# Optimization experiments

Hardware: AMD Instinct MI355X
Metric: run time of the kernel (lower is better)

Reference implementation:

```python
import jax, jax.numpy as jnp
import numpy as np

N_NODES, N_EDGES, FEA_DIM, H_DIM, N_LAYER, N_GRAPHS, LABEL_DIM = 50000, 600000, 128, 256, 3, 256, 2


def setup_inputs() -> dict:
    key = jax.random.key(0)
    ks = jax.random.split(key, 8)
    x = jax.random.normal(ks[0], (N_NODES, FEA_DIM), jnp.float32)
    edge_index = jax.random.randint(ks[1], (2, N_EDGES), 0, N_NODES, dtype=jnp.int64)
    batch = jnp.sort(jax.random.randint(ks[2], (N_NODES,), 0, N_GRAPHS, dtype=jnp.int64))
    Wg = jax.random.normal(ks[3], (N_LAYER, FEA_DIM, FEA_DIM), jnp.float32) / np.sqrt(FEA_DIM)
    bg = jnp.zeros((N_LAYER, FEA_DIM), jnp.float32)
    w1 = jax.random.normal(ks[4], (FEA_DIM, H_DIM), jnp.float32) / np.sqrt(FEA_DIM)
    b1 = jnp.zeros((H_DIM,), jnp.float32)
    w2 = jax.random.normal(ks[5], (H_DIM, LABEL_DIM), jnp.float32) / np.sqrt(H_DIM)
    b2 = jnp.zeros((LABEL_DIM,), jnp.float32)
    return dict(x=x, Wg=Wg, bg=bg, w1=w1, b1=b1, w2=w2, b2=b2,
                edge_index=edge_index, batch=batch)


def reference(x, Wg, bg, w1, b1, w2, b2, edge_index, batch):
    N = x.shape[0]
    # --- GCN normalization with self-loops (PyG GCNConv default) ---
    loop = jnp.arange(N, dtype=edge_index.dtype)
    src = jnp.concatenate([edge_index[0], loop])  # [E+N]
    dst = jnp.concatenate([edge_index[1], loop])
    deg = jax.ops.segment_sum(jnp.ones_like(src, x.dtype), dst, num_segments=N)
    dinv = jnp.where(deg > 0, jax.lax.rsqrt(jnp.maximum(deg, 1.0)), 0.0)
    norm = dinv[src] * dinv[dst]  # [E+N]
    # --- stacked GCNConv + ReLU ---
    for l in range(Wg.shape[0]):
        h = x @ Wg[l]                              # [N, D] linear transform
        msg = h[src] * norm[:, None]               # gather + edge scale
        x = jax.ops.segment_sum(msg, dst, num_segments=N) + bg[l]  # scatter-add
        x = jax.nn.relu(x)
    # --- global mean pool over graphs ---
    sums = jax.ops.segment_sum(x, batch, num_segments=N_GRAPHS)
    counts = jax.ops.segment_sum(jnp.ones((N, 1), x.dtype), batch, num_segments=N_GRAPHS)
    pooled = sums / jnp.maximum(counts, 1.0)       # [G, D]
    # --- MLP head ---
    h = jax.nn.relu(pooled @ w1 + b1)
    return h @ w2 + b2                             # [G, label_dim]
```

## Files before the change

kernel.cpp:

```cpp
#include <hip/hip_runtime.h>
#include <hip/hip_bf16.h>

#define N_NODES 50000
#define N_EDGES 600000
#define FEA_DIM 128
#define H_DIM 256
#define N_LAYER 3
#define N_GRAPHS 256
#define LABEL_DIM 2

#define SCAN_NB ((N_NODES + 255) / 256)


__global__ __launch_bounds__(256) void k_count(const int* __restrict__ dst, int* __restrict__ counts) {
    int e = blockIdx.x * 256 + threadIdx.x;
    if (e < N_EDGES) atomicAdd(&counts[dst[e]], 1);
}

__global__ __launch_bounds__(256) void k_partial(const int* __restrict__ counts, int* __restrict__ partial) {
    int g = blockIdx.x * 256 + threadIdx.x;
    int v = (g < N_NODES) ? counts[g] : 0;
#pragma unroll
    for (int off = 32; off > 0; off >>= 1) v += __shfl_down(v, off);
    __shared__ int ws[4];
    int lane = threadIdx.x & 63, wid = threadIdx.x >> 6;
    if (lane == 0) ws[wid] = v;
    __syncthreads();
    if (threadIdx.x == 0) partial[blockIdx.x] = ws[0] + ws[1] + ws[2] + ws[3];
}

__global__ __launch_bounds__(256) void k_rowptr(const int* __restrict__ counts, const int* __restrict__ partial,
                                                int* __restrict__ row_ptr, float* __restrict__ dinv) {
    __shared__ int sp[256];
    __shared__ int s[256];
    int tid = threadIdx.x;
    sp[tid] = (tid < SCAN_NB) ? partial[tid] : 0;
    __syncthreads();
#pragma unroll
    for (int off = 1; off < 256; off <<= 1) {
        int t = (tid >= off) ? sp[tid - off] : 0;
        __syncthreads();
        sp[tid] += t;
        __syncthreads();
    }
    int block_off = (blockIdx.x == 0) ? 0 : sp[blockIdx.x - 1];

    int g = blockIdx.x * 256 + tid;
    int c = (g < N_NODES) ? counts[g] : 0;
    s[tid] = c;
    __syncthreads();
#pragma unroll
    for (int off = 1; off < 256; off <<= 1) {
        int t = (tid >= off) ? s[tid - off] : 0;
        __syncthreads();
        s[tid] += t;
        __syncthreads();
    }
    if (g < N_NODES) {
        row_ptr[g] = block_off + s[tid] - c;
        dinv[g] = rsqrtf((float)c + 1.0f);
    }
    if (blockIdx.x == 0 && tid == 0) row_ptr[N_NODES] = sp[SCAN_NB - 1];
}

__global__ __launch_bounds__(256) void k_fill(const int* __restrict__ src, const int* __restrict__ dst,
                                              const int* __restrict__ row_ptr, int* __restrict__ cursor,
                                              int* __restrict__ col) {
    int e = blockIdx.x * 256 + threadIdx.x;
    if (e >= N_EDGES) return;
    int s = src[e], d = dst[e];
    int p = row_ptr[d] + atomicAdd(&cursor[d], 1);
    col[p] = s;
}


__global__ __launch_bounds__(256) void k_gemm(const float* __restrict__ X, const float* __restrict__ W,
                                              float* __restrict__ H, int M) {
    __shared__ float a_s[32][132];
    __shared__ float b_s[32][128];
    const int tid = threadIdx.x;
    const int row_g = tid >> 4;
    const int col_g = tid & 15;
    const int row_base = blockIdx.x * 128;
    float acc[8][8] = {};

    for (int kt = 0; kt < 4; ++kt) {
        const int k0 = kt * 32;
#pragma unroll
        for (int j = 0; j < 4; ++j) {
            int id = tid + j * 256;
            int m = id >> 3;
            int kq = (id & 7) << 2;
            float4 v = make_float4(0.f, 0.f, 0.f, 0.f);
            int gr = row_base + m;
            if (gr < M) v = *(const float4*)(X + gr * 128 + k0 + kq);
            a_s[kq + 0][m] = v.x; a_s[kq + 1][m] = v.y;
            a_s[kq + 2][m] = v.z; a_s[kq + 3][m] = v.w;
        }
#pragma unroll
        for (int j = 0; j < 4; ++j) {
            int id = tid + j * 256;
            int k = id >> 5;
            int n = (id & 31) << 2;
            *(float4*)(&b_s[k][n]) = *(const float4*)(W + (k0 + k) * 128 + n);
        }
        __syncthreads();
#pragma unroll 8
        for (int k = 0; k < 32; ++k) {
            float4 a0 = *(const float4*)(&a_s[k][row_g * 8]);
            float4 a1 = *(const float4*)(&a_s[k][row_g * 8 + 4]);
            float4 b0 = *(const float4*)(&b_s[k][col_g * 4]);
            float4 b1 = *(const float4*)(&b_s[k][64 + col_g * 4]);
            float av[8] = {a0.x, a0.y, a0.z, a0.w, a1.x, a1.y, a1.z, a1.w};
            float bv[8] = {b0.x, b0.y, b0.z, b0.w, b1.x, b1.y, b1.z, b1.w};
#pragma unroll
            for (int i = 0; i < 8; ++i)
#pragma unroll
                for (int jj = 0; jj < 8; ++jj) acc[i][jj] += av[i] * bv[jj];
        }
        __syncthreads();
    }
#pragma unroll
    for (int i = 0; i < 8; ++i) {
        int gr = row_base + row_g * 8 + i;
        if (gr < M) {
            float4 o0 = {acc[i][0], acc[i][1], acc[i][2], acc[i][3]};
            float4 o1 = {acc[i][4], acc[i][5], acc[i][6], acc[i][7]};
            *(float4*)(H + gr * 128 + col_g * 4) = o0;
            *(float4*)(H + gr * 128 + 64 + col_g * 4) = o1;
        }
    }
}


__global__ __launch_bounds__(256) void k_agg(const float* __restrict__ H, const float* __restrict__ bgl,
                                             const int* __restrict__ row_ptr, const int* __restrict__ col,
                                             const float* __restrict__ dinv,
                                             float* __restrict__ Xo) {
    const int i = (blockIdx.x * 256 + threadIdx.x) >> 5;
    if (i >= N_NODES) return;
    const int fl = threadIdx.x & 31;
    const float4* H4 = (const float4*)H;
    const float di = dinv[i];
    float4 h = H4[i * 32 + fl];
    float4 acc;
    const float wself = di * di;
    acc.x = h.x * wself; acc.y = h.y * wself; acc.z = h.z * wself; acc.w = h.w * wself;
    const int p0 = row_ptr[i], p1 = row_ptr[i + 1];
    for (int base = p0; base < p1; base += 32) {
        int m = p1 - base; if (m > 32) m = 32;
        int sc = 0; float wc = 0.f;
        if (fl < m) { sc = col[base + fl]; wc = dinv[sc] * di; }
        for (int j = 0; j < m; j += 8) {
            int cnt = m - j; if (cnt > 8) cnt = 8;
            float4 hbuf[8]; float wbuf[8];
#pragma unroll
            for (int t = 0; t < 8; ++t) {
                if (t < cnt) {
                    int s = __shfl(sc, j + t, 32);
                    wbuf[t] = __shfl(wc, j + t, 32);
                    hbuf[t] = H4[(size_t)s * 32 + fl];
                }
            }
#pragma unroll
            for (int t = 0; t < 8; ++t) {
                if (t < cnt) {
                    acc.x += hbuf[t].x * wbuf[t];
                    acc.y += hbuf[t].y * wbuf[t];
                    acc.z += hbuf[t].z * wbuf[t];
                    acc.w += hbuf[t].w * wbuf[t];
                }
            }
        }
    }
    float4 b = ((const float4*)bgl)[fl];
    float4 o;
    o.x = fmaxf(acc.x + b.x, 0.f);
    o.y = fmaxf(acc.y + b.y, 0.f);
    o.z = fmaxf(acc.z + b.z, 0.f);
    o.w = fmaxf(acc.w + b.w, 0.f);
    ((float4*)Xo)[i * 32 + fl] = o;
}


__global__ __launch_bounds__(256) void k_poolmlp(const float* __restrict__ X, const int* __restrict__ batch,
                                                 const float* __restrict__ w1, const float* __restrict__ b1,
                                                 const float* __restrict__ w2, const float* __restrict__ b2,
                                                 float* __restrict__ out) {
    __shared__ int s_lo, s_hi;
    __shared__ float red[256];
    __shared__ float xs[128];
    __shared__ float hs[256];
    int g = blockIdx.x, tid = threadIdx.x;
    if (tid == 0) {
        int lo = 0, hi = N_NODES;
        while (lo < hi) { int mid = (lo + hi) >> 1; if (batch[mid] < g) lo = mid + 1; else hi = mid; }
        s_lo = lo;
        int lo2 = lo, hi2 = N_NODES;
        while (lo2 < hi2) { int mid = (lo2 + hi2) >> 1; if (batch[mid] < g + 1) lo2 = mid + 1; else hi2 = mid; }
        s_hi = lo2;
    }
    __syncthreads();
    int lo = s_lo, hi = s_hi;
    int f = tid & 127, half = tid >> 7;
    float acc = 0.f;
    for (int r = lo + half; r < hi; r += 2) acc += X[r * 128 + f];
    red[tid] = acc;
    __syncthreads();
    if (tid < 128) {
        int cnt = hi - lo;
        xs[tid] = (red[tid] + red[tid + 128]) / (float)(cnt > 0 ? cnt : 1);
    }
    __syncthreads();
    float a1 = b1[tid];
#pragma unroll 8
    for (int k = 0; k < 128; ++k) a1 += xs[k] * w1[k * H_DIM + tid];
    hs[tid] = fmaxf(a1, 0.f);
    __syncthreads();
    int j = tid >> 7, t2 = tid & 127;
    float p = hs[t2] * w2[t2 * LABEL_DIM + j] + hs[t2 + 128] * w2[(t2 + 128) * LABEL_DIM + j];
    red[tid] = p;
    __syncthreads();
    for (int s2 = 64; s2 > 0; s2 >>= 1) {
        if (t2 < s2) red[tid] += red[tid + s2];
        __syncthreads();
    }
    if (t2 == 0) out[g * LABEL_DIM + j] = red[tid] + b2[j];
}


extern "C" void kernel_launch(void* const* d_in, const int* in_sizes, int n_in,
                              void* d_out, int out_size, void* d_ws, size_t ws_size,
                              hipStream_t stream) {
    const float* x   = (const float*)d_in[0];
    const float* Wg  = (const float*)d_in[1];
    const float* bg  = (const float*)d_in[2];
    const float* w1  = (const float*)d_in[3];
    const float* b1  = (const float*)d_in[4];
    const float* w2  = (const float*)d_in[5];
    const float* b2  = (const float*)d_in[6];
    const int* eidx  = (const int*)d_in[7];
    const int* batch = (const int*)d_in[8];
    float* out = (float*)d_out;

    const int* src = eidx;
    const int* dst = eidx + N_EDGES;

    char* ws = (char*)d_ws;
    size_t off = 0;
    float* A = (float*)(ws + off); off += (size_t)N_NODES * FEA_DIM * 4;
    float* B = (float*)(ws + off); off += (size_t)N_NODES * FEA_DIM * 4;
    int*   col = (int*)(ws + off); off += (size_t)N_EDGES * 4;
    int*   row_ptr = (int*)(ws + off); off += 200704;
    int*   cursor  = (int*)(ws + off); off += 200704;
    int*   counts  = (int*)(ws + off); off += 200704;
    float* dinv    = (float*)(ws + off); off += 200704;
    int*   partial = (int*)(ws + off); off += 4096;

    hipMemsetAsync(cursor, 0, 2 * 200704, stream);
    k_count<<<(N_EDGES + 255) / 256, 256, 0, stream>>>(dst, counts);
    k_partial<<<SCAN_NB, 256, 0, stream>>>(counts, partial);
    k_rowptr<<<SCAN_NB, 256, 0, stream>>>(counts, partial, row_ptr, dinv);
    k_fill<<<(N_EDGES + 255) / 256, 256, 0, stream>>>(src, dst, row_ptr, cursor, col);

    const float* cur = x;
    for (int l = 0; l < N_LAYER; ++l) {
        k_gemm<<<(N_NODES + 127) / 128, 256, 0, stream>>>(cur, Wg + (size_t)l * FEA_DIM * FEA_DIM, B, N_NODES);
        k_agg<<<(N_NODES + 7) / 8, 256, 0, stream>>>(B, bg + (size_t)l * FEA_DIM, row_ptr, col, dinv, A);
        cur = A;
    }
    k_poolmlp<<<N_GRAPHS, 256, 0, stream>>>(A, batch, w1, b1, w2, b2, out);
}
```

Baseline: 420.5 us.

## Fuse first GEMM with degree count and software-pipeline neighbor gathers in aggregation

The first layer's GEMM and the edge degree-count atomics now run in one launch, with blocks split by index, so the two independent stages overlap. The cursor reset moves into the row-pointer kernel, which shrinks the memset. The aggregation kernel double-buffers neighbor feature loads, issuing the next group of 8 gathers before accumulating the previous group, to hide gather latency. This costs extra registers and may lower occupancy in k_agg.

Measured after the change: 409.5 us. -2.6%, faster.

```diff
diff --git a/kernel.cpp b/kernel.cpp
--- a/kernel.cpp
+++ b/kernel.cpp
@@ -10,78 +10,18 @@
 #define LABEL_DIM 2
 
 #define SCAN_NB ((N_NODES + 255) / 256)
-
-
-__global__ __launch_bounds__(256) void k_count(const int* __restrict__ dst, int* __restrict__ counts) {
-    int e = blockIdx.x * 256 + threadIdx.x;
-    if (e < N_EDGES) atomicAdd(&counts[dst[e]], 1);
-}
-
-__global__ __launch_bounds__(256) void k_partial(const int* __restrict__ counts, int* __restrict__ partial) {
-    int g = blockIdx.x * 256 + threadIdx.x;
-    int v = (g < N_NODES) ? counts[g] : 0;
-#pragma unroll
-    for (int off = 32; off > 0; off >>= 1) v += __shfl_down(v, off);
-    __shared__ int ws[4];
-    int lane = threadIdx.x & 63, wid = threadIdx.x >> 6;
-    if (lane == 0) ws[wid] = v;
-    __syncthreads();
-    if (threadIdx.x == 0) partial[blockIdx.x] = ws[0] + ws[1] + ws[2] + ws[3];
-}
-
-__global__ __launch_bounds__(256) void k_rowptr(const int* __restrict__ counts, const int* __restrict__ partial,
-                                                int* __restrict__ row_ptr, float* __restrict__ dinv) {
-    __shared__ int sp[256];
-    __shared__ int s[256];
-    int tid = threadIdx.x;
-    sp[tid] = (tid < SCAN_NB) ? partial[tid] : 0;
-    __syncthreads();
-#pragma unroll
-    for (int off = 1; off < 256; off <<= 1) {
-        int t = (tid >= off) ? sp[tid - off] : 0;
-        __syncthreads();
-        sp[tid] += t;
-        __syncthreads();
-    }
-    int block_off = (blockIdx.x == 0) ? 0 : sp[blockIdx.x - 1];
-
-    int g = blockIdx.x * 256 + tid;
-    int c = (g < N_NODES) ? counts[g] : 0;
-    s[tid] = c;
-    __syncthreads();
-#pragma unroll
-    for (int off = 1; off < 256; off <<= 1) {
-        int t = (tid >= off) ? s[tid - off] : 0;
-        __syncthreads();
-        s[tid] += t;
-        __syncthreads();
-    }
-    if (g < N_NODES) {
-        row_ptr[g] = block_off + s[tid] - c;
-        dinv[g] = rsqrtf((float)c + 1.0f);
-    }
-    if (blockIdx.x == 0 && tid == 0) row_ptr[N_NODES] = sp[SCAN_NB - 1];
-}
-
-__global__ __launch_bounds__(256) void k_fill(const int* __restrict__ src, const int* __restrict__ dst,
-                                              const int* __restrict__ row_ptr, int* __restrict__ cursor,
-                                              int* __restrict__ col) {
-    int e = blockIdx.x * 256 + threadIdx.x;
-    if (e >= N_EDGES) return;
-    int s = src[e], d = dst[e];
-    int p = row_ptr[d] + atomicAdd(&cursor[d], 1);
-    col[p] = s;
-}
-
-
-__global__ __launch_bounds__(256) void k_gemm(const float* __restrict__ X, const float* __restrict__ W,
-                                              float* __restrict__ H, int M) {
+#define GEMM_NB ((N_NODES + 127) / 128)
+#define COUNT_NB ((N_EDGES + 255) / 256)
+
+
+__device__ __forceinline__ void gemm_body(const float* __restrict__ X, const float* __restrict__ W,
+                                          float* __restrict__ H, int M, int tile) {
     __shared__ float a_s[32][132];
     __shared__ float b_s[32][128];
     const int tid = threadIdx.x;
     const int row_g = tid >> 4;
     const int col_g = tid & 15;
-    const int row_base = blockIdx.x * 128;
+    const int row_base = tile * 128;
     float acc[8][8] = {};
 
     for (int kt = 0; kt < 4; ++kt) {
@@ -132,6 +72,81 @@
     }
 }
 
+__global__ __launch_bounds__(256) void k_gemm(const float* __restrict__ X, const float* __restrict__ W,
+                                              float* __restrict__ H, int M) {
+    gemm_body(X, W, H, M, blockIdx.x);
+}
+
+__global__ __launch_bounds__(256) void k_gemm0_count(const float* __restrict__ X, const float* __restrict__ W,
+                                                     float* __restrict__ H,
+                                                     const int* __restrict__ dst, int* __restrict__ counts) {
+    if (blockIdx.x < GEMM_NB) {
+        gemm_body(X, W, H, N_NODES, blockIdx.x);
+    } else {
+        int e = (blockIdx.x - GEMM_NB) * 256 + threadIdx.x;
+        if (e < N_EDGES) atomicAdd(&counts[dst[e]], 1);
+    }
+}
+
+
+__global__ __launch_bounds__(256) void k_partial(const int* __restrict__ counts, int* __restrict__ partial) {
+    int g = blockIdx.x * 256 + threadIdx.x;
+    int v = (g < N_NODES) ? counts[g] : 0;
+#pragma unroll
+    for (int off = 32; off > 0; off >>= 1) v += __shfl_down(v, off);
+    __shared__ int ws[4];
+    int lane = threadIdx.x & 63, wid = threadIdx.x >> 6;
+    if (lane == 0) ws[wid] = v;
+    __syncthreads();
+    if (threadIdx.x == 0) partial[blockIdx.x] = ws[0] + ws[1] + ws[2] + ws[3];
+}
+
+__global__ __launch_bounds__(256) void k_rowptr(const int* __restrict__ counts, const int* __restrict__ partial,
+                                                int* __restrict__ row_ptr, float* __restrict__ dinv,
+                                                int* __restrict__ cursor) {
+    __shared__ int sp[256];
+    __shared__ int s[256];
+    int tid = threadIdx.x;
+    sp[tid] = (tid < SCAN_NB) ? partial[tid] : 0;
+    __syncthreads();
+#pragma unroll
+    for (int off = 1; off < 256; off <<= 1) {
+        int t = (tid >= off) ? sp[tid - off] : 0;
+        __syncthreads();
+        sp[tid] += t;
+        __syncthreads();
+    }
+    int block_off = (blockIdx.x == 0) ? 0 : sp[blockIdx.x - 1];
+
+    int g = blockIdx.x * 256 + tid;
+    int c = (g < N_NODES) ? counts[g] : 0;
+    s[tid] = c;
+    __syncthreads();
+#pragma unroll
+    for (int off = 1; off < 256; off <<= 1) {
+        int t = (tid >= off) ? s[tid - off] : 0;
+        __syncthreads();
+        s[tid] += t;
+        __syncthreads();
+    }
+    if (g < N_NODES) {
+        row_ptr[g] = block_off + s[tid] - c;
+        dinv[g] = rsqrtf((float)c + 1.0f);
+        cursor[g] = 0;
+    }
+    if (blockIdx.x == 0 && tid == 0) row_ptr[N_NODES] = sp[SCAN_NB - 1];
+}
+
+__global__ __launch_bounds__(256) void k_fill(const int* __restrict__ src, const int* __restrict__ dst,
+                                              const int* __restrict__ row_ptr, int* __restrict__ cursor,
+                                              int* __restrict__ col) {
+    int e = blockIdx.x * 256 + threadIdx.x;
+    if (e >= N_EDGES) return;
+    int s = src[e], d = dst[e];
+    int p = row_ptr[d] + atomicAdd(&cursor[d], 1);
+    col[p] = s;
+}
+
 
 __global__ __launch_bounds__(256) void k_agg(const float* __restrict__ H, const float* __restrict__ bgl,
                                              const int* __restrict__ row_ptr, const int* __restrict__ col,
@@ -142,34 +157,54 @@
     const int fl = threadIdx.x & 31;
     const float4* H4 = (const float4*)H;
     const float di = dinv[i];
-    float4 h = H4[i * 32 + fl];
-    float4 acc;
+    float4 h = H4[(size_t)i * 32 + fl];
     const float wself = di * di;
-    acc.x = h.x * wself; acc.y = h.y * wself; acc.z = h.z * wself; acc.w = h.w * wself;
+    float4 acc = make_float4(h.x * wself, h.y * wself, h.z * wself, h.w * wself);
     const int p0 = row_ptr[i], p1 = row_ptr[i + 1];
     for (int base = p0; base < p1; base += 32) {
         int m = p1 - base; if (m > 32) m = 32;
         int sc = 0; float wc = 0.f;
         if (fl < m) { sc = col[base + fl]; wc = dinv[sc] * di; }
-        for (int j = 0; j < m; j += 8) {
-            int cnt = m - j; if (cnt > 8) cnt = 8;
-            float4 hbuf[8]; float wbuf[8];
+        float4 hb0[8], hb1[8]; float wb0[8], wb1[8];
+        int cnt0 = (m < 8) ? m : 8;
+#pragma unroll
+        for (int t = 0; t < 8; ++t) {
+            if (t < cnt0) {
+                int s = __shfl(sc, t, 32);
+                wb0[t] = __shfl(wc, t, 32);
+                hb0[t] = H4[(size_t)s * 32 + fl];
+            }
+        }
+        for (int j = 8; j < m; j += 8) {
+            int cnt1 = m - j; if (cnt1 > 8) cnt1 = 8;
 #pragma unroll
             for (int t = 0; t < 8; ++t) {
-                if (t < cnt) {
+                if (t < cnt1) {
                     int s = __shfl(sc, j + t, 32);
-                    wbuf[t] = __shfl(wc, j + t, 32);
-                    hbuf[t] = H4[(size_t)s * 32 + fl];
+                    wb1[t] = __shfl(wc, j + t, 32);
+                    hb1[t] = H4[(size_t)s * 32 + fl];
                 }
             }
 #pragma unroll
             for (int t = 0; t < 8; ++t) {
-                if (t < cnt) {
-                    acc.x += hbuf[t].x * wbuf[t];
-                    acc.y += hbuf[t].y * wbuf[t];
-                    acc.z += hbuf[t].z * wbuf[t];
-                    acc.w += hbuf[t].w * wbuf[t];
+                if (t < cnt0) {
+                    acc.x += hb0[t].x * wb0[t];
+                    acc.y += hb0[t].y * wb0[t];
+                    acc.z += hb0[t].z * wb0[t];
+                    acc.w += hb0[t].w * wb0[t];
                 }
+            }
+#pragma unroll
+            for (int t = 0; t < 8; ++t) { hb0[t] = hb1[t]; wb0[t] = wb1[t]; }
+            cnt0 = cnt1;
+        }
+#pragma unroll
+        for (int t = 0; t < 8; ++t) {
+            if (t < cnt0) {
+                acc.x += hb0[t].x * wb0[t];
+                acc.y += hb0[t].y * wb0[t];
+                acc.z += hb0[t].z * wb0[t];
+                acc.w += hb0[t].w * wb0[t];
             }
         }
     }
@@ -179,7 +214,7 @@
     o.y = fmaxf(acc.y + b.y, 0.f);
     o.z = fmaxf(acc.z + b.z, 0.f);
     o.w = fmaxf(acc.w + b.w, 0.f);
-    ((float4*)Xo)[i * 32 + fl] = o;
+    ((float4*)Xo)[(size_t)i * 32 + fl] = o;
 }
 
 
@@ -257,17 +292,16 @@
     float* dinv    = (float*)(ws + off); off += 200704;
     int*   partial = (int*)(ws + off); off += 4096;
 
-    hipMemsetAsync(cursor, 0, 2 * 200704, stream);
-    k_count<<<(N_EDGES + 255) / 256, 256, 0, stream>>>(dst, counts);
+    hipMemsetAsync(counts, 0, 200704, stream);
+    k_gemm0_count<<<GEMM_NB + COUNT_NB, 256, 0, stream>>>(x, Wg, B, dst, counts);
     k_partial<<<SCAN_NB, 256, 0, stream>>>(counts, partial);
-    k_rowptr<<<SCAN_NB, 256, 0, stream>>>(counts, partial, row_ptr, dinv);
-    k_fill<<<(N_EDGES + 255) / 256, 256, 0, stream>>>(src, dst, row_ptr, cursor, col);
-
-    const float* cur = x;
-    for (int l = 0; l < N_LAYER; ++l) {
-        k_gemm<<<(N_NODES + 127) / 128, 256, 0, stream>>>(cur, Wg + (size_t)l * FEA_DIM * FEA_DIM, B, N_NODES);
+    k_rowptr<<<SCAN_NB, 256, 0, stream>>>(counts, partial, row_ptr, dinv, cursor);
+    k_fill<<<COUNT_NB, 256, 0, stream>>>(src, dst, row_ptr, cursor, col);
+
+    k_agg<<<(N_NODES + 7) / 8, 256, 0, stream>>>(B, bg + 0 * FEA_DIM, row_ptr, col, dinv, A);
+    for (int l = 1; l < N_LAYER; ++l) {
+        k_gemm<<<GEMM_NB, 256, 0, stream>>>(A, Wg + (size_t)l * FEA_DIM * FEA_DIM, B, N_NODES);
         k_agg<<<(N_NODES + 7) / 8, 256, 0, stream>>>(B, bg + (size_t)l * FEA_DIM, row_ptr, col, dinv, A);
-        cur = A;
     }
     k_poolmlp<<<N_GRAPHS, 256, 0, stream>>>(A, batch, w1, b1, w2, b2, out);
 }
```
